# Performance work log

Hardware: AMD Instinct MI355X
Metric: run time of the kernel (lower is better)

The kernel has to match this reference:

```python
import jax, jax.numpy as jnp
import numpy as np
import math

D_MODEL = 1024
D_K = 256
B, T = 4, 4096

def setup_inputs() -> dict:
    key = jax.random.key(0)
    ks = jax.random.split(key, 7)
    s = 1.0 / math.sqrt(D_MODEL)
    return {
        "inputs": jax.random.normal(ks[0], (B, T, D_MODEL), dtype=jnp.float32),
        "Wq": jax.random.uniform(ks[1], (D_MODEL, D_K), jnp.float32, -s, s),
        "bq": jax.random.uniform(ks[2], (D_K,), jnp.float32, -s, s),
        "Wk": jax.random.uniform(ks[3], (D_MODEL, D_K), jnp.float32, -s, s),
        "bk": jax.random.uniform(ks[4], (D_K,), jnp.float32, -s, s),
        "Wv": jax.random.uniform(ks[5], (D_MODEL, D_K), jnp.float32, -s, s),
        "bv": jax.random.uniform(ks[6], (D_K,), jnp.float32, -s, s),
    }

def reference(inputs, Wq, bq, Wk, bk, Wv, bv):
    q = inputs @ Wq + bq                      # [B,T,d_k]
    k = inputs @ Wk + bk
    v = inputs @ Wv + bv
    scores = jnp.einsum('btd,bsd->bts', q, k)  # [B,T,T]
    Tdim = inputs.shape[1]
    causal = jnp.tril(jnp.ones((Tdim, Tdim), dtype=bool))
    # faithful to original: mask with -1e9 BEFORE dividing by sqrt(d_k)
    scores = jnp.where(causal[None], scores, jnp.float32(-1e9))
    attn = jax.nn.softmax(scores / math.sqrt(D_K), axis=-1)
    return jnp.einsum('bts,bsd->btd', attn, v)
```

## Files before the change

### kernel.cpp

```cpp
#include <hip/hip_runtime.h>
#include <stdint.h>

typedef uint16_t u16;
typedef uint32_t u32;
typedef float    f32x4  __attribute__((ext_vector_type(4)));
typedef short    bf16x8 __attribute__((ext_vector_type(8)));
typedef u32      u32x4  __attribute__((ext_vector_type(4)));
typedef u16      u16x8  __attribute__((ext_vector_type(8)));
typedef u16      u16x4  __attribute__((ext_vector_type(4)));

#define MFMA16(a, b, c) __builtin_amdgcn_mfma_f32_16x16x32_bf16((a), (b), (c), 0, 0, 0)


__device__ __forceinline__ u16 f2bf(float f) {
  u32 x = __float_as_uint(f);
  return (u16)((x + 0x7FFFu + ((x >> 16) & 1u)) >> 16);
}

__global__ __launch_bounds__(256) void cvt_x_kernel(const float* __restrict__ X,
                                                    u16* __restrict__ Xb) {
  int i = (blockIdx.x * 256 + threadIdx.x) * 8;
  f32x4 a = *(const f32x4*)(X + i);
  f32x4 b = *(const f32x4*)(X + i + 4);
  u16x8 o;
  o[0] = f2bf(a[0]); o[1] = f2bf(a[1]); o[2] = f2bf(a[2]); o[3] = f2bf(a[3]);
  o[4] = f2bf(b[0]); o[5] = f2bf(b[1]); o[6] = f2bf(b[2]); o[7] = f2bf(b[3]);
  *(u16x8*)(Xb + i) = o;
}

__global__ __launch_bounds__(256) void cvt_w_kernel(const float* __restrict__ Wq,
                                                    const float* __restrict__ Wk,
                                                    const float* __restrict__ Wv,
                                                    u16* __restrict__ Wt) {
  int idx = blockIdx.x * 256 + threadIdx.x;
  int m = idx >> 18;
  int n = (idx >> 10) & 255;
  int k = idx & 1023;
  const float* W = (m == 0) ? Wq : (m == 1) ? Wk : Wv;
  Wt[idx] = f2bf(W[k * 256 + n]);
}

__global__ __launch_bounds__(256) void qkv_gemm_kernel(
    const u16* __restrict__ Xb, const u16* __restrict__ Wt,
    const float* __restrict__ bq, const float* __restrict__ bk, const float* __restrict__ bv,
    u16* __restrict__ Qb, u16* __restrict__ Kb, u16* __restrict__ Vtb) {
  __shared__ __align__(16) char sm[32768];
  const int tid = threadIdx.x;
  const int wid = tid >> 6, lane = tid & 63, g = lane >> 4, lr = lane & 15;
  const int wr = wid >> 1, wc = wid & 1;
  const int m0 = blockIdx.x * 128, n0 = blockIdx.y * 128, z = blockIdx.z;
  const u16* W = Wt + z * 262144;

  f32x4 acc[4][4];
#pragma unroll
  for (int mi = 0; mi < 4; ++mi)
#pragma unroll
    for (int ni = 0; ni < 4; ++ni) {
      acc[mi][ni][0] = 0.f; acc[mi][ni][1] = 0.f; acc[mi][ni][2] = 0.f; acc[mi][ni][3] = 0.f;
    }

  for (int k0 = 0; k0 < 1024; k0 += 64) {
    __syncthreads();
#pragma unroll
    for (int r = 0; r < 4; ++r) {
      int ch = r * 256 + tid;
      int row = ch >> 3, c = ch & 7;
      u32x4 vx = *(const u32x4*)(Xb + (size_t)(m0 + row) * 1024 + k0 + c * 8);
      *(u32x4*)(sm + row * 128 + 16 * (c ^ (row & 7))) = vx;
      u32x4 vw = *(const u32x4*)(W + (size_t)(n0 + row) * 1024 + k0 + c * 8);
      *(u32x4*)(sm + 16384 + row * 128 + 16 * (c ^ (row & 7))) = vw;
    }
    __syncthreads();
#pragma unroll
    for (int kk = 0; kk < 2; ++kk) {
      bf16x8 af[4], bfr[4];
#pragma unroll
      for (int mi = 0; mi < 4; ++mi) {
        int row = wr * 64 + mi * 16 + lr;
        af[mi] = *(const bf16x8*)(sm + row * 128 + 16 * ((kk * 4 + g) ^ (row & 7)));
      }
#pragma unroll
      for (int ni = 0; ni < 4; ++ni) {
        int row = wc * 64 + ni * 16 + lr;
        bfr[ni] = *(const bf16x8*)(sm + 16384 + row * 128 + 16 * ((kk * 4 + g) ^ (row & 7)));
      }
#pragma unroll
      for (int mi = 0; mi < 4; ++mi)
#pragma unroll
        for (int ni = 0; ni < 4; ++ni)
          acc[mi][ni] = MFMA16(af[mi], bfr[ni], acc[mi][ni]);
    }
  }

  const float* bias = (z == 0) ? bq : (z == 1) ? bk : bv;
  if (z < 2) {
    u16* O = (z == 0) ? Qb : Kb;
    const float qscale = (z == 0) ? 0.0625f : 1.0f;
#pragma unroll
    for (int ni = 0; ni < 4; ++ni) {
      int col = n0 + wc * 64 + ni * 16 + lr;
      float bb = bias[col];
#pragma unroll
      for (int mi = 0; mi < 4; ++mi)
#pragma unroll
        for (int j = 0; j < 4; ++j) {
          int row = m0 + wr * 64 + mi * 16 + 4 * g + j;
          O[(size_t)row * 256 + col] = f2bf((acc[mi][ni][j] + bb) * qscale);
        }
    }
  } else {
    __syncthreads();
#pragma unroll
    for (int ni = 0; ni < 4; ++ni) {
      int cl = wc * 64 + ni * 16 + lr;
      float bb = bias[n0 + cl];
#pragma unroll
      for (int mi = 0; mi < 4; ++mi)
#pragma unroll
        for (int j = 0; j < 4; ++j) {
          int rl = wr * 64 + mi * 16 + 4 * g + j;
          *(u16*)(sm + cl * 256 + rl * 2) = f2bf(acc[mi][ni][j] + bb);
        }
    }
    __syncthreads();
    int bidx = m0 >> 12, tb = m0 & 4095;
#pragma unroll
    for (int r = 0; r < 8; ++r) {
      int ch = r * 256 + tid;
      int cl = ch >> 4, tp = ch & 15;
      u32x4 v = *(const u32x4*)(sm + cl * 256 + tp * 16);
      *(u32x4*)(Vtb + (size_t)bidx * 1048576 + (size_t)(n0 + cl) * 4096 + tb + tp * 8) = v;
    }
  }
}

__global__ __launch_bounds__(256) void flash_kernel(
    const u16* __restrict__ Qb, const u16* __restrict__ Kb,
    const u16* __restrict__ Vtb, u16* __restrict__ Opart, float2* __restrict__ ML,
    int s, int gx) {
  __shared__ __align__(16) char sm[69632];
  const int tid = threadIdx.x, wid = tid >> 6, lane = tid & 63, g = lane >> 4, lr = lane & 15;
  const int b = blockIdx.y;
  const int G = 64 >> s;
  int x = blockIdx.x, g4 = 0;
  while (g4 < G - 1 && x >= (((g4 + 1) * (g4 + 2)) << (s - 1))) ++g4;
  const int local = x - ((g4 * (g4 + 1)) << (s - 1));
  const int qq = local / (g4 + 1);
  const int sc = local - qq * (g4 + 1);
  const int qb = (g4 << s) + qq;
  const int t0 = qb * 64;
  const int w0 = t0 + wid * 16;
  const int C = 64 << s;
  const int sbase = sc * C;

  bf16x8 qf[8];
  const u16* Qrow = Qb + (size_t)(b * 4096 + w0 + lr) * 256;
#pragma unroll
  for (int kk = 0; kk < 8; ++kk) qf[kk] = *(const bf16x8*)(Qrow + kk * 32 + g * 8);

  f32x4 o[16];
#pragma unroll
  for (int n = 0; n < 16; ++n) { o[n][0] = 0.f; o[n][1] = 0.f; o[n][2] = 0.f; o[n][3] = 0.f; }
  float m_ = -1e30f, l_ = 0.f;

  const u16* Kbase = Kb + (size_t)b * 4096 * 256;
  const u16* Vbase = Vtb + (size_t)b * 1048576;

  const int nto = min(C >> 6, (t0 + 64 - sbase) >> 6);
  for (int ot = 0; ot < nto; ++ot) {
    const int os0 = sbase + ot * 64;
    __syncthreads();
#pragma unroll
    for (int half = 0; half < 2; ++half) {
      const int sh = os0 + 32 * half;
      char* kb = sm + half * 16384;
      char* vb = sm + 32768 + half * 16384;
#pragma unroll
      for (int r = 0; r < 4; ++r) {
        int ch = r * 256 + tid;
        int srow = ch >> 5, c = ch & 31;
        u32x4 v = *(const u32x4*)(Kbase + (size_t)(sh + srow) * 256 + c * 8);
        *(u32x4*)(kb + srow * 512 + 16 * (c ^ (srow & 7))) = v;
        int d = ch >> 2, c2 = ch & 3;
        u32x4 v2 = *(const u32x4*)(Vbase + (size_t)d * 4096 + sh + c2 * 8);
        *(u32x4*)(vb + d * 64 + 16 * (c2 ^ ((d >> 1) & 3))) = v2;
      }
    }
    __syncthreads();

#pragma unroll 1
    for (int half = 0; half < 2; ++half) {
      const int s0 = os0 + 32 * half;
      if (s0 > w0 + 15) break;
      const char* kb = sm + half * 16384;
      const char* vb = sm + 32768 + half * 16384;

      f32x4 sa[2];
#pragma unroll
      for (int ni = 0; ni < 2; ++ni) { sa[ni][0] = 0.f; sa[ni][1] = 0.f; sa[ni][2] = 0.f; sa[ni][3] = 0.f; }
#pragma unroll
      for (int ni = 0; ni < 2; ++ni) {
        int srw = ni * 16 + lr;
#pragma unroll
        for (int kk = 0; kk < 8; ++kk) {
          bf16x8 kf = *(const bf16x8*)(kb + srw * 512 + 16 * ((kk * 4 + g) ^ (srw & 7)));
          sa[ni] = MFMA16(kf, qf[kk], sa[ni]);
        }
      }
      const int t = w0 + lr;
      if (s0 + 31 > w0) {
#pragma unroll
        for (int ni = 0; ni < 2; ++ni)
#pragma unroll
          for (int j = 0; j < 4; ++j) {
            int ss = s0 + ni * 16 + 4 * g + j;
            if (t < ss) sa[ni][j] = -1e30f;
          }
      }
      float mt = fmaxf(fmaxf(fmaxf(sa[0][0], sa[0][1]), fmaxf(sa[0][2], sa[0][3])),
                       fmaxf(fmaxf(sa[1][0], sa[1][1]), fmaxf(sa[1][2], sa[1][3])));
      mt = fmaxf(mt, __shfl_xor(mt, 16, 64));
      mt = fmaxf(mt, __shfl_xor(mt, 32, 64));
      if (__any(mt > m_ + 8.0f)) {
        float mn = fmaxf(m_, mt);
        float scale = __expf(m_ - mn);
        m_ = mn;
        l_ *= scale;
#pragma unroll
        for (int n = 0; n < 16; ++n)
#pragma unroll
          for (int j = 0; j < 4; ++j) o[n][j] *= scale;
      }
#pragma unroll
      for (int ni = 0; ni < 2; ++ni)
#pragma unroll
        for (int j = 0; j < 4; ++j) sa[ni][j] = __expf(sa[ni][j] - m_);
      float su = (sa[0][0] + sa[0][1]) + (sa[0][2] + sa[0][3]) +
                 (sa[1][0] + sa[1][1]) + (sa[1][2] + sa[1][3]);
      su += __shfl_xor(su, 16, 64);
      su += __shfl_xor(su, 32, 64);
      l_ += su;
#pragma unroll
      for (int ni = 0; ni < 2; ++ni)
#pragma unroll
        for (int j = 0; j < 4; ++j) {
          int c = ni * 2 + (g >> 1);
          *(u16*)(sm + 65536 + wid * 1024 + lr * 64 + 16 * (c ^ (lr & 3)) + (4 * (g & 1) + j) * 2) =
              f2bf(sa[ni][j]);
        }
      asm volatile("s_waitcnt lgkmcnt(0)" ::: "memory");
      bf16x8 pf = *(const bf16x8*)(sm + 65536 + wid * 1024 + lr * 64 + 16 * (g ^ (lr & 3)));
#pragma unroll
      for (int n = 0; n < 16; ++n) {
        int d = n * 16 + lr;
        bf16x8 vf = *(const bf16x8*)(vb + d * 64 + 16 * (g ^ ((d >> 1) & 3)));
        o[n] = MFMA16(vf, pf, o[n]);
      }
    }
  }

  u16* Orow = Opart + ((size_t)(b * gx + blockIdx.x) * 64 + wid * 16) * 256;
#pragma unroll
  for (int n = 0; n < 16; ++n) {
    u16x4 pk;
    pk[0] = f2bf(o[n][0]); pk[1] = f2bf(o[n][1]); pk[2] = f2bf(o[n][2]); pk[3] = f2bf(o[n][3]);
    *(u16x4*)(Orow + lr * 256 + n * 16 + 4 * g) = pk;
  }
  if (lane < 16) {
    float2 ml; ml.x = m_; ml.y = l_;
    ML[(size_t)(b * gx + blockIdx.x) * 64 + wid * 16 + lane] = ml;
  }
}

__global__ __launch_bounds__(256) void combine_kernel(const u16* __restrict__ Opart,
                                                      const float2* __restrict__ ML,
                                                      float* __restrict__ out,
                                                      int s, int gx) {
  const int wid = threadIdx.x >> 6, lane = threadIdx.x & 63;
  const int rg = blockIdx.x * 4 + wid;
  const int b = rg >> 12, t = rg & 4095;
  const int qb = t >> 6;
  const int gg = qb >> s, qq = qb & ((1 << s) - 1);
  const int n = gg + 1;
  const size_t base = (size_t)(b * gx) + ((gg * (gg + 1)) << (s - 1)) + qq * (gg + 1);
  const int tl = t & 63;
  float mv[16], lv[16], w[16];
  float M = -1e30f;
#pragma unroll
  for (int sc = 0; sc < 16; ++sc)
    if (sc < n) {
      float2 ml = ML[(base + sc) * 64 + tl];
      mv[sc] = ml.x; lv[sc] = ml.y;
      M = fmaxf(M, ml.x);
    }
  float L = 0.f;
#pragma unroll
  for (int sc = 0; sc < 16; ++sc)
    if (sc < n) { w[sc] = __expf(mv[sc] - M); L += w[sc] * lv[sc]; }
  const float inv = 1.0f / L;
  const int c0 = lane * 4;
  float a0 = 0.f, a1 = 0.f, a2 = 0.f, a3 = 0.f;
#pragma unroll
  for (int sc = 0; sc < 16; ++sc)
    if (sc < n) {
      u16x4 v = *(const u16x4*)(Opart + ((base + sc) * 64 + tl) * 256 + c0);
      a0 += w[sc] * __uint_as_float((u32)v[0] << 16);
      a1 += w[sc] * __uint_as_float((u32)v[1] << 16);
      a2 += w[sc] * __uint_as_float((u32)v[2] << 16);
      a3 += w[sc] * __uint_as_float((u32)v[3] << 16);
    }
  f32x4 r; r[0] = a0 * inv; r[1] = a1 * inv; r[2] = a2 * inv; r[3] = a3 * inv;
  *(f32x4*)(out + (size_t)rg * 256 + c0) = r;
}

extern "C" void kernel_launch(void* const* d_in, const int* in_sizes, int n_in,
                              void* d_out, int out_size, void* d_ws, size_t ws_size,
                              hipStream_t stream) {
  const float* X  = (const float*)d_in[0];
  const float* Wq = (const float*)d_in[1];
  const float* bq = (const float*)d_in[2];
  const float* Wk = (const float*)d_in[3];
  const float* bk = (const float*)d_in[4];
  const float* Wv = (const float*)d_in[5];
  const float* bv = (const float*)d_in[6];
  float* out = (float*)d_out;
  char* ws = (char*)d_ws;

  const size_t OFF_WT  = 33554432;
  const size_t OFF_Q   = OFF_WT + 1572864;
  const size_t OFF_K   = OFF_Q + 8388608;
  const size_t OFF_VT  = OFF_K + 8388608;
  const size_t PREFIX  = OFF_VT + 8388608;

  const size_t NEEDED_A = PREFIX + 589824 + 37748736;
  const size_t NEEDED_B = PREFIX + 327680;
  if (ws_size < NEEDED_B) return;

  u16* Xb  = (u16*)ws;
  u16* Wt  = (u16*)(ws + OFF_WT);
  u16* Qb  = (u16*)(ws + OFF_Q);
  u16* Kb  = (u16*)(ws + OFF_K);
  u16* Vtb = (u16*)(ws + OFF_VT);

  int s, gx;
  u16* Opart;
  float2* ML;
  if (ws_size >= NEEDED_A) {
    s = 3; gx = 288;
    ML = (float2*)(ws + PREFIX);
    Opart = (u16*)(ws + PREFIX + 589824);
  } else {
    s = 4; gx = 160;
    ML = (float2*)(ws + PREFIX);
    Opart = (u16*)ws;
  }

  cvt_x_kernel<<<8192, 256, 0, stream>>>(X, Xb);
  cvt_w_kernel<<<3072, 256, 0, stream>>>(Wq, Wk, Wv, Wt);
  qkv_gemm_kernel<<<dim3(128, 2, 3), 256, 0, stream>>>(Xb, Wt, bq, bk, bv, Qb, Kb, Vtb);
  flash_kernel<<<dim3(gx, 4), 256, 0, stream>>>(Qb, Kb, Vtb, Opart, ML, s, gx);
  combine_kernel<<<4096, 256, 0, stream>>>(Opart, ML, out, s, gx);
}
```

Before: 176.8 us.

## Fuse X conversion into QKV GEMM and use 512-thread flash blocks with XCD mapping

Drops the standalone fp32-to-bf16 conversion kernel for X and converts X inside the QKV GEMM's shared-memory load, which removes a full write and re-read of the bf16 copy of X. The flash kernel moves to 512 threads per block covering 128 query rows, so each loaded K/V tile is shared by eight waves instead of four. Blocks are launched on a 1D grid whose index is remapped so that each batch lands on particular XCDs, aiming for better L2 locality. The combine kernel's partial indexing is updated to the new 128-row split layout. The risks are that the GEMM now reads twice as many bytes of X per tile, and that the larger blocks with more LDS may lower occupancy.

```diff
diff --git a/kernel.cpp b/kernel.cpp
--- a/kernel.cpp
+++ b/kernel.cpp
@@ -15,17 +15,6 @@
 __device__ __forceinline__ u16 f2bf(float f) {
   u32 x = __float_as_uint(f);
   return (u16)((x + 0x7FFFu + ((x >> 16) & 1u)) >> 16);
-}
-
-__global__ __launch_bounds__(256) void cvt_x_kernel(const float* __restrict__ X,
-                                                    u16* __restrict__ Xb) {
-  int i = (blockIdx.x * 256 + threadIdx.x) * 8;
-  f32x4 a = *(const f32x4*)(X + i);
-  f32x4 b = *(const f32x4*)(X + i + 4);
-  u16x8 o;
-  o[0] = f2bf(a[0]); o[1] = f2bf(a[1]); o[2] = f2bf(a[2]); o[3] = f2bf(a[3]);
-  o[4] = f2bf(b[0]); o[5] = f2bf(b[1]); o[6] = f2bf(b[2]); o[7] = f2bf(b[3]);
-  *(u16x8*)(Xb + i) = o;
 }
 
 __global__ __launch_bounds__(256) void cvt_w_kernel(const float* __restrict__ Wq,
@@ -41,7 +30,7 @@
 }
 
 __global__ __launch_bounds__(256) void qkv_gemm_kernel(
-    const u16* __restrict__ Xb, const u16* __restrict__ Wt,
+    const float* __restrict__ X, const u16* __restrict__ Wt,
     const float* __restrict__ bq, const float* __restrict__ bk, const float* __restrict__ bv,
     u16* __restrict__ Qb, u16* __restrict__ Kb, u16* __restrict__ Vtb) {
   __shared__ __align__(16) char sm[32768];
@@ -65,8 +54,13 @@
     for (int r = 0; r < 4; ++r) {
       int ch = r * 256 + tid;
       int row = ch >> 3, c = ch & 7;
-      u32x4 vx = *(const u32x4*)(Xb + (size_t)(m0 + row) * 1024 + k0 + c * 8);
-      *(u32x4*)(sm + row * 128 + 16 * (c ^ (row & 7))) = vx;
+      const float* xp = X + (size_t)(m0 + row) * 1024 + k0 + c * 8;
+      f32x4 xa = *(const f32x4*)xp;
+      f32x4 xb = *(const f32x4*)(xp + 4);
+      u16x8 xc;
+      xc[0] = f2bf(xa[0]); xc[1] = f2bf(xa[1]); xc[2] = f2bf(xa[2]); xc[3] = f2bf(xa[3]);
+      xc[4] = f2bf(xb[0]); xc[5] = f2bf(xb[1]); xc[6] = f2bf(xb[2]); xc[7] = f2bf(xb[3]);
+      *(u16x8*)(sm + row * 128 + 16 * (c ^ (row & 7))) = xc;
       u32x4 vw = *(const u32x4*)(W + (size_t)(n0 + row) * 1024 + k0 + c * 8);
       *(u32x4*)(sm + 16384 + row * 128 + 16 * (c ^ (row & 7))) = vw;
     }
@@ -134,21 +128,24 @@
   }
 }
 
-__global__ __launch_bounds__(256) void flash_kernel(
+__global__ __launch_bounds__(512, 4) void flash_kernel(
     const u16* __restrict__ Qb, const u16* __restrict__ Kb,
     const u16* __restrict__ Vtb, u16* __restrict__ Opart, float2* __restrict__ ML,
     int s, int gx) {
-  __shared__ __align__(16) char sm[69632];
+  __shared__ __align__(16) char sm[73728];
   const int tid = threadIdx.x, wid = tid >> 6, lane = tid & 63, g = lane >> 4, lr = lane & 15;
-  const int b = blockIdx.y;
-  const int G = 64 >> s;
-  int x = blockIdx.x, g4 = 0;
-  while (g4 < G - 1 && x >= (((g4 + 1) * (g4 + 2)) << (s - 1))) ++g4;
-  const int local = x - ((g4 * (g4 + 1)) << (s - 1));
+  const int xcd = blockIdx.x & 7;
+  const int b = xcd >> 1;
+  const int i = ((blockIdx.x >> 3) << 1) + (xcd & 1);
+  const int QG = 1 << (s - 1);
+  const int NG = 32 >> (s - 1);
+  int g4 = 0;
+  while (g4 < NG - 1 && i >= (((g4 + 1) * (g4 + 2)) << (s - 2))) ++g4;
+  const int local = i - ((g4 * (g4 + 1)) << (s - 2));
   const int qq = local / (g4 + 1);
   const int sc = local - qq * (g4 + 1);
-  const int qb = (g4 << s) + qq;
-  const int t0 = qb * 64;
+  const int qb = g4 * QG + qq;
+  const int t0 = qb * 128;
   const int w0 = t0 + wid * 16;
   const int C = 64 << s;
   const int sbase = sc * C;
@@ -166,7 +163,7 @@
   const u16* Kbase = Kb + (size_t)b * 4096 * 256;
   const u16* Vbase = Vtb + (size_t)b * 1048576;
 
-  const int nto = min(C >> 6, (t0 + 64 - sbase) >> 6);
+  const int nto = min(C >> 6, (t0 + 128 - sbase) >> 6);
   for (int ot = 0; ot < nto; ++ot) {
     const int os0 = sbase + ot * 64;
     __syncthreads();
@@ -176,8 +173,8 @@
       char* kb = sm + half * 16384;
       char* vb = sm + 32768 + half * 16384;
 #pragma unroll
-      for (int r = 0; r < 4; ++r) {
-        int ch = r * 256 + tid;
+      for (int rr = 0; rr < 2; ++rr) {
+        int ch = rr * 512 + tid;
         int srow = ch >> 5, c = ch & 31;
         u32x4 v = *(const u32x4*)(Kbase + (size_t)(sh + srow) * 256 + c * 8);
         *(u32x4*)(kb + srow * 512 + 16 * (c ^ (srow & 7))) = v;
@@ -259,7 +256,7 @@
     }
   }
 
-  u16* Orow = Opart + ((size_t)(b * gx + blockIdx.x) * 64 + wid * 16) * 256;
+  u16* Orow = Opart + ((size_t)(b * gx + i) * 128 + wid * 16) * 256;
 #pragma unroll
   for (int n = 0; n < 16; ++n) {
     u16x4 pk;
@@ -268,7 +265,7 @@
   }
   if (lane < 16) {
     float2 ml; ml.x = m_; ml.y = l_;
-    ML[(size_t)(b * gx + blockIdx.x) * 64 + wid * 16 + lane] = ml;
+    ML[(size_t)(b * gx + i) * 128 + wid * 16 + lane] = ml;
   }
 }
 
@@ -279,31 +276,31 @@
   const int wid = threadIdx.x >> 6, lane = threadIdx.x & 63;
   const int rg = blockIdx.x * 4 + wid;
   const int b = rg >> 12, t = rg & 4095;
-  const int qb = t >> 6;
-  const int gg = qb >> s, qq = qb & ((1 << s) - 1);
+  const int qb = t >> 7;
+  const int gg = qb >> (s - 1), qq = qb & ((1 << (s - 1)) - 1);
   const int n = gg + 1;
-  const size_t base = (size_t)(b * gx) + ((gg * (gg + 1)) << (s - 1)) + qq * (gg + 1);
-  const int tl = t & 63;
-  float mv[16], lv[16], w[16];
+  const size_t base = (size_t)(b * gx) + ((gg * (gg + 1)) << (s - 2)) + qq * (gg + 1);
+  const int tl = t & 127;
+  float mv[8], lv[8], w[8];
   float M = -1e30f;
 #pragma unroll
-  for (int sc = 0; sc < 16; ++sc)
+  for (int sc = 0; sc < 8; ++sc)
     if (sc < n) {
-      float2 ml = ML[(base + sc) * 64 + tl];
+      float2 ml = ML[(base + sc) * 128 + tl];
       mv[sc] = ml.x; lv[sc] = ml.y;
       M = fmaxf(M, ml.x);
     }
   float L = 0.f;
 #pragma unroll
-  for (int sc = 0; sc < 16; ++sc)
+  for (int sc = 0; sc < 8; ++sc)
     if (sc < n) { w[sc] = __expf(mv[sc] - M); L += w[sc] * lv[sc]; }
   const float inv = 1.0f / L;
   const int c0 = lane * 4;
   float a0 = 0.f, a1 = 0.f, a2 = 0.f, a3 = 0.f;
 #pragma unroll
-  for (int sc = 0; sc < 16; ++sc)
+  for (int sc = 0; sc < 8; ++sc)
     if (sc < n) {
-      u16x4 v = *(const u16x4*)(Opart + ((base + sc) * 64 + tl) * 256 + c0);
+      u16x4 v = *(const u16x4*)(Opart + ((base + sc) * 128 + tl) * 256 + c0);
       a0 += w[sc] * __uint_as_float((u32)v[0] << 16);
       a1 += w[sc] * __uint_as_float((u32)v[1] << 16);
       a2 += w[sc] * __uint_as_float((u32)v[2] << 16);
@@ -336,7 +333,6 @@
   const size_t NEEDED_B = PREFIX + 327680;
   if (ws_size < NEEDED_B) return;
 
-  u16* Xb  = (u16*)ws;
   u16* Wt  = (u16*)(ws + OFF_WT);
   u16* Qb  = (u16*)(ws + OFF_Q);
   u16* Kb  = (u16*)(ws + OFF_K);
@@ -346,18 +342,17 @@
   u16* Opart;
   float2* ML;
   if (ws_size >= NEEDED_A) {
-    s = 3; gx = 288;
+    s = 3; gx = 144;
     ML = (float2*)(ws + PREFIX);
     Opart = (u16*)(ws + PREFIX + 589824);
   } else {
-    s = 4; gx = 160;
+    s = 4; gx = 80;
     ML = (float2*)(ws + PREFIX);
     Opart = (u16*)ws;
   }
 
-  cvt_x_kernel<<<8192, 256, 0, stream>>>(X, Xb);
   cvt_w_kernel<<<3072, 256, 0, stream>>>(Wq, Wk, Wv, Wt);
-  qkv_gemm_kernel<<<dim3(128, 2, 3), 256, 0, stream>>>(Xb, Wt, bq, bk, bv, Qb, Kb, Vtb);
-  flash_kernel<<<dim3(gx, 4), 256, 0, stream>>>(Qb, Kb, Vtb, Opart, ML, s, gx);
+  qkv_gemm_kernel<<<dim3(128, 2, 3), 256, 0, stream>>>(X, Wt, bq, bk, bv, Qb, Kb, Vtb);
+  flash_kernel<<<4 * gx, 512, 0, stream>>>(Qb, Kb, Vtb, Opart, ML, s, gx);
   combine_kernel<<<4096, 256, 0, stream>>>(Opart, ML, out, s, gx);
 }
```

New measurement: 196.0 us. 1.11x slower.
